# Performance work log

Measured on AMD Instinct MI355X. Metric: run time of the kernel, lower is better.

The kernel has to match this reference:

```python
import jax, jax.numpy as jnp
import numpy as np

D_MODEL = 1024
EXPAND = 2
HEADDIM = 64
D_STATE = 128
D_CONV = 4
D_INNER = EXPAND * D_MODEL          # 2048
NHEADS = D_INNER // HEADDIM         # 32
CONV_DIM = D_INNER + 2 * D_STATE    # x, B, C share the depthwise conv
EPS = 1e-5


def setup_inputs() -> dict:
    key = jax.random.key(0)
    ks = jax.random.split(key, 8)
    d_in_proj = 2 * D_INNER + 2 * D_STATE + NHEADS
    x = jax.random.normal(ks[0], (2, 2048, D_MODEL), jnp.float32)
    W_in = jax.random.normal(ks[1], (D_MODEL, d_in_proj), jnp.float32) * (D_MODEL ** -0.5)
    conv_w = jax.random.normal(ks[2], (CONV_DIM, D_CONV), jnp.float32) * 0.2
    conv_b = jnp.zeros((CONV_DIM,), jnp.float32)
    # dt init: softplus(dt_bias) in [1e-3, 1e-1]  (inverse-softplus init, as in mamba_ssm)
    dt = jnp.exp(jax.random.uniform(ks[3], (NHEADS,), jnp.float32,
                                    minval=np.log(1e-3), maxval=np.log(1e-1)))
    dt_bias = dt + jnp.log(-jnp.expm1(-dt))
    A_log = jnp.log(jax.random.uniform(ks[4], (NHEADS,), jnp.float32, minval=1.0, maxval=16.0))
    D = jnp.ones((NHEADS,), jnp.float32)
    norm_w = jnp.ones((D_INNER,), jnp.float32)
    W_out = jax.random.normal(ks[5], (D_INNER, D_MODEL), jnp.float32) * (D_INNER ** -0.5)
    return dict(x=x, W_in=W_in, conv_w=conv_w, conv_b=conv_b, dt_bias=dt_bias,
                A_log=A_log, D=D, norm_w=norm_w, W_out=W_out)


def _causal_depthwise_conv(u, w, b):
    # u: (B, L, C), w: (C, K) depthwise, causal (pad K-1 on the left)
    B, L, C = u.shape
    up = jnp.pad(u, ((0, 0), (D_CONV - 1, 0), (0, 0)))
    y = b
    for k in range(D_CONV):
        y = y + up[:, k:k + L, :] * w[:, k]
    return y


def _rms(v):
    return v * jax.lax.rsqrt(jnp.mean(v * v, axis=-1, keepdims=True) + EPS)


def reference(x, W_in, conv_w, conv_b, dt_bias, A_log, D, norm_w, W_out):
    b, l, _ = x.shape
    zxbcdt = x @ W_in                                  # (b, l, 2*d_inner + 2*d_state + nheads)
    z = zxbcdt[..., :D_INNER]
    xBC = zxbcdt[..., D_INNER:D_INNER + CONV_DIM]
    dt = jax.nn.softplus(zxbcdt[..., -NHEADS:] + dt_bias)   # (b, l, h)
    xBC = jax.nn.silu(_causal_depthwise_conv(xBC, conv_w, conv_b))
    xs = xBC[..., :D_INNER].reshape(b, l, NHEADS, HEADDIM)  # (b, l, h, p)
    Bm = xBC[..., D_INNER:D_INNER + D_STATE]                 # (b, l, n)
    Cm = xBC[..., D_INNER + D_STATE:]                        # (b, l, n)
    A = -jnp.exp(A_log)                                      # (h,)
    decay = jnp.exp(dt * A)                                  # (b, l, h)

    def step(h, inp):
        dec_t, dt_t, x_t, B_t, C_t = inp   # (b,h) (b,h) (b,h,p) (b,n) (b,n)
        h = h * dec_t[:, :, None, None] + (dt_t[:, :, None] * x_t)[..., None] * B_t[:, None, None, :]
        y_t = jnp.einsum('bhpn,bn->bhp', h, C_t)
        return h, y_t

    h0 = jnp.zeros((b, NHEADS, HEADDIM, D_STATE), x.dtype)
    xs_t = (decay.transpose(1, 0, 2), dt.transpose(1, 0, 2),
            xs.transpose(1, 0, 2, 3), Bm.transpose(1, 0, 2), Cm.transpose(1, 0, 2))
    _, ys = jax.lax.scan(step, h0, xs_t)                     # ys: (l, b, h, p)
    y = ys.transpose(1, 0, 2, 3) + D[None, None, :, None] * xs
    y = y.reshape(b, l, D_INNER)
    # gated RMSNorm (RMSNormGated in mamba_ssm), then out projection
    y = _rms(y * jax.nn.silu(z)) * norm_w
    out = y @ W_out                                          # (b, l, d_model)
    # wrapper: post RMSNorm (weight freshly initialized to ones) + residual
    return _rms(out) + x
```

## Files before the change

### kernel.cpp

```cpp
#include <hip/hip_runtime.h>
#include <hip/hip_bf16.h>

#define DMODEL 1024
#define DI     2048
#define DSTATE 128
#define NH     32
#define HD     64
#define CONVD  2304
#define LSEQ   2048
#define BATCH  2
#define DPROJ  4384
#define NPAD   4480
#define EPSV   1e-5f
#define QCH    128
#define NCH    16

#define AS1 __attribute__((address_space(1)))
#define AS3 __attribute__((address_space(3)))

typedef __attribute__((ext_vector_type(8))) short bf16x8;
typedef __attribute__((ext_vector_type(4))) float f32x4;

union U4 { ushort4 u; __hip_bfloat16 h[4]; };

__device__ __forceinline__ float bf2f(unsigned short u) {
  union { unsigned int i; float f; } c; c.i = ((unsigned)u) << 16; return c.f;
}
__device__ __forceinline__ ushort4 pack4(float x0, float x1, float x2, float x3) {
  U4 p;
  p.h[0] = __float2bfloat16(x0); p.h[1] = __float2bfloat16(x1);
  p.h[2] = __float2bfloat16(x2); p.h[3] = __float2bfloat16(x3);
  return p.u;
}

__device__ __forceinline__ bf16x8 ldsfrag(const __hip_bfloat16* base, int row, int ke) {
  int byte = row * 256 + ke * 2;
  byte ^= (row & 7) << 4;
  return *reinterpret_cast<const bf16x8*>(reinterpret_cast<const char*>(base) + byte);
}
__device__ __forceinline__ void ldswr4(__hip_bfloat16* base, int row, int col4, ushort4 v) {
  int byte = row * 256 + col4 * 2;
  byte ^= (row & 7) << 4;
  *reinterpret_cast<ushort4*>(reinterpret_cast<char*>(base) + byte) = v;
}
__device__ __forceinline__ void ldswr8(__hip_bfloat16* base, int row, int colElem,
                                       unsigned lo, unsigned hi) {
  int byte = row * 256 + colElem * 2;
  byte ^= (row & 7) << 4;
  uint2 v; v.x = lo; v.y = hi;
  *reinterpret_cast<uint2*>(reinterpret_cast<char*>(base) + byte) = v;
}
__device__ __forceinline__ bf16x8 frag32(const __hip_bfloat16* base, int row, int g) {
  int byte = row * 64 + (((g ^ (row >> 1)) & 3) << 4);
  return *reinterpret_cast<const bf16x8*>(reinterpret_cast<const char*>(base) + byte);
}
__device__ __forceinline__ bf16x8 frag64s(const __hip_bfloat16* base, int row, int ch) {
  int byte = row * 128 + ((ch ^ (row & 7)) << 4);
  return *reinterpret_cast<const bf16x8*>(reinterpret_cast<const char*>(base) + byte);
}

__device__ __forceinline__ void quadtr(unsigned a01, unsigned a23, int ql,
                                       unsigned& w01, unsigned& w23) {
  unsigned y01 = __shfl_xor((int)a01, 1), y23 = __shfl_xor((int)a23, 1);
  unsigned c01 = (ql & 1) ? ((y01 >> 16) | (a01 & 0xFFFF0000u))
                          : ((a01 & 0xFFFFu) | (y01 << 16));
  unsigned c23 = (ql & 1) ? ((y23 >> 16) | (a23 & 0xFFFF0000u))
                          : ((a23 & 0xFFFFu) | (y23 << 16));
  unsigned d01 = __shfl_xor((int)c01, 2), d23 = __shfl_xor((int)c23, 2);
  w01 = (ql & 2) ? d23 : c01;
  w23 = (ql & 2) ? c23 : d01;
}


__global__ void f32_to_bf16_kernel(const float* __restrict__ in,
                                   __hip_bfloat16* __restrict__ out, int n4) {
  int i = blockIdx.x * 256 + threadIdx.x;
  if (i >= n4) return;
  float4 v = reinterpret_cast<const float4*>(in)[i];
  reinterpret_cast<ushort4*>(out)[i] = pack4(v.x, v.y, v.z, v.w);
}

__global__ void transpose_f32_bf16(const float* __restrict__ in,
                                   __hip_bfloat16* __restrict__ out,
                                   int R, int C, int Cpad) {
  __shared__ float tile[32][33];
  int n0 = blockIdx.x * 32, k0 = blockIdx.y * 32;
  int tx = threadIdx.x, ty = threadIdx.y;
#pragma unroll
  for (int j = 0; j < 32; j += 8) {
    int k = k0 + ty + j, n = n0 + tx;
    tile[ty + j][tx] = (n < C) ? in[(size_t)k * C + n] : 0.f;
  }
  __syncthreads();
#pragma unroll
  for (int j = 0; j < 32; j += 8) {
    int n = n0 + ty + j, k = k0 + tx;
    if (n < Cpad) out[(size_t)n * R + k] = __float2bfloat16(tile[tx][ty + j]);
  }
}


__global__ __launch_bounds__(512, 2)
void gemm256_bt(const __hip_bfloat16* __restrict__ A,
                const __hip_bfloat16* __restrict__ Bt,
                __hip_bfloat16* __restrict__ C, int K) {
  __shared__ __hip_bfloat16 smA[2][256 * 64];
  __shared__ __hip_bfloat16 smB[2][256 * 64];
  const int xcd = blockIdx.x & 7;
  const int i = blockIdx.x >> 3;
  const int bm = (xcd * 2 + (i & 1)) * 256;
  const int bn = (i >> 1) * 256;
  const int tid = threadIdx.x;
  const int w = tid >> 6, lane = tid & 63;
  const int wm = w >> 2, wn = w & 3;
  const int fr = lane & 15, g = lane >> 4;
  const int srow = w * 8 + (lane >> 3);
  const int scol = ((lane & 7) ^ (lane >> 3)) * 8;

  f32x4 acc[8][4];
#pragma unroll
  for (int m = 0; m < 8; ++m)
#pragma unroll
    for (int n = 0; n < 4; ++n) acc[m][n] = (f32x4){0.f, 0.f, 0.f, 0.f};

  const __hip_bfloat16* aS = A + (size_t)(bm + srow) * K + scol;
  const __hip_bfloat16* bS = Bt + (size_t)(bn + srow) * K + scol;

  auto STAGE = [&](int buf, int kt) {
    const int k0 = kt << 6;
#pragma unroll
    for (int j = 0; j < 4; ++j) {
      __builtin_amdgcn_global_load_lds((const AS1 void*)(aS + (size_t)(j * 64) * K + k0),
                                       (AS3 void*)(&smA[buf][(j * 64 + w * 8) * 64]), 16, 0, 0);
      __builtin_amdgcn_global_load_lds((const AS1 void*)(bS + (size_t)(j * 64) * K + k0),
                                       (AS3 void*)(&smB[buf][(j * 64 + w * 8) * 64]), 16, 0, 0);
    }
  };

  STAGE(0, 0);
  int cur = 0;
  const int nt = K >> 6;
  for (int kt = 0; kt < nt; ++kt) {
    if (kt + 1 < nt) {
      STAGE(cur ^ 1, kt + 1);
      asm volatile("s_waitcnt vmcnt(8)" ::: "memory");
    } else {
      asm volatile("s_waitcnt vmcnt(0)" ::: "memory");
    }
    __builtin_amdgcn_s_barrier();
    __builtin_amdgcn_s_setprio(1);
#pragma unroll
    for (int ks = 0; ks < 2; ++ks) {
      const int ch = ks * 4 + g;
      bf16x8 af[8], bfv[4];
#pragma unroll
      for (int m = 0; m < 8; ++m)
        af[m] = frag64s(&smA[cur][0], wm * 128 + m * 16 + fr, ch);
#pragma unroll
      for (int n = 0; n < 4; ++n)
        bfv[n] = frag64s(&smB[cur][0], wn * 64 + n * 16 + fr, ch);
#pragma unroll
      for (int m = 0; m < 8; ++m)
#pragma unroll
        for (int n = 0; n < 4; ++n)
          acc[m][n] = __builtin_amdgcn_mfma_f32_16x16x32_bf16(af[m], bfv[n], acc[m][n], 0, 0, 0);
    }
    __builtin_amdgcn_s_setprio(0);
    __builtin_amdgcn_s_barrier();
    cur ^= 1;
  }

  const int rb = g * 4;
#pragma unroll
  for (int m = 0; m < 8; ++m)
#pragma unroll
    for (int n = 0; n < 4; ++n) {
      int row = bm + wm * 128 + m * 16 + rb;
      int col = bn + wn * 64 + n * 16 + fr;
      __hip_bfloat16* cp = C + (size_t)row * NPAD + col;
#pragma unroll
      for (int j = 0; j < 4; ++j)
        cp[(size_t)j * NPAD] = __float2bfloat16(acc[m][n][j]);
    }
}


template <int OUTMODE, int SPLITK>
__global__ __launch_bounds__(256, 4)
void gemm_bt3(const __hip_bfloat16* __restrict__ A,
              const __hip_bfloat16* __restrict__ Bt,
              void* __restrict__ Cout0, float* __restrict__ Cout1,
              float* __restrict__ dtraw,
              int M, int N, int K, int bnOff, int NT) {
  __shared__ __hip_bfloat16 smA[2][128 * 32];
  __shared__ __hip_bfloat16 smB[2][128 * 32];
  int bb = blockIdx.x;
  int s = 0;
  if constexpr (SPLITK == 2) { s = bb >> 8; bb &= 255; }
  int bm, bn;
  if (NT == 0) {
    const int xcd = bb & 7;
    const int i = bb >> 3;
    bm = ((xcd << 2) + (i & 3)) * 128;
    bn = bnOff + (i >> 2) * 128;
  } else {
    bm = (bb / NT) * 128;
    bn = bnOff + (bb % NT) * 128;
  }
  const int Kp = (SPLITK == 2) ? (K >> 1) : K;
  const int kbase = s * Kp;
  const int t = threadIdx.x;
  const int w = t >> 6, lane = t & 63;
  const int wr = (w >> 1) * 64, wc = (w & 1) * 64;
  const int fr = lane & 15, g = lane >> 4;
  const int srow = lane >> 2;
  const int scol = ((lane & 3) ^ ((lane >> 3) & 3)) * 8;

  f32x4 acc[4][4];
#pragma unroll
  for (int m = 0; m < 4; ++m)
#pragma unroll
    for (int n = 0; n < 4; ++n) acc[m][n] = (f32x4){0.f, 0.f, 0.f, 0.f};

  const __hip_bfloat16* aSrc = A + (size_t)(bm + srow) * K + kbase + scol;
  const __hip_bfloat16* bSrc = Bt + (size_t)(bn + srow) * K + kbase + scol;

  auto STAGE = [&](int buf, int k0) {
#pragma unroll
    for (int j = 0; j < 2; ++j) {
      int ro = w * 32 + j * 16;
      __builtin_amdgcn_global_load_lds((const AS1 void*)(aSrc + (size_t)ro * K + k0),
                                       (AS3 void*)(&smA[buf][ro * 32]), 16, 0, 0);
      __builtin_amdgcn_global_load_lds((const AS1 void*)(bSrc + (size_t)ro * K + k0),
                                       (AS3 void*)(&smB[buf][ro * 32]), 16, 0, 0);
    }
  };

  STAGE(0, 0);
  __syncthreads();
  const int nt = Kp >> 5;
  int cur = 0;
  for (int kt = 0; kt < nt; ++kt) {
    if (kt + 1 < nt) STAGE(cur ^ 1, (kt + 1) << 5);
    bf16x8 af[4], bfv[4];
#pragma unroll
    for (int m = 0; m < 4; ++m) af[m] = frag32(&smA[cur][0], wr + m * 16 + fr, g);
#pragma unroll
    for (int n = 0; n < 4; ++n) bfv[n] = frag32(&smB[cur][0], wc + n * 16 + fr, g);
#pragma unroll
    for (int m = 0; m < 4; ++m)
#pragma unroll
      for (int n = 0; n < 4; ++n)
        acc[m][n] = __builtin_amdgcn_mfma_f32_16x16x32_bf16(af[m], bfv[n], acc[m][n], 0, 0, 0);
    __syncthreads();
    cur ^= 1;
  }

  const int r4 = g * 4;
  const int cn = lane & 15;
#pragma unroll
  for (int m = 0; m < 4; ++m)
#pragma unroll
    for (int n = 0; n < 4; ++n) {
      int row = bm + wr + m * 16 + r4;
      int col = bn + wc + n * 16 + cn;
      if constexpr (OUTMODE == 0) {
        float* cp = (float*)(s ? Cout1 : (float*)Cout0) + (size_t)row * N + col;
#pragma unroll
        for (int j = 0; j < 4; ++j) cp[(size_t)j * N] = acc[m][n][j];
      } else {
        __hip_bfloat16* cp = (__hip_bfloat16*)Cout0 + (size_t)row * N + col;
#pragma unroll
        for (int j = 0; j < 4; ++j) {
          float v = acc[m][n][j];
          cp[(size_t)j * N] = __float2bfloat16(v);
          if (col >= DI + CONVD && col < DPROJ)
            dtraw[(size_t)(row + j) * NH + (col - (DI + CONVD))] = v;
        }
      }
    }
}


__global__ __launch_bounds__(256)
void chunk_stats_kernel(const float* __restrict__ dtraw, const float* __restrict__ dt_bias,
                        const float* __restrict__ A_log,
                        float* __restrict__ csb, float* __restrict__ dtc,
                        float* __restrict__ swb, float* __restrict__ cumdecb,
                        float* __restrict__ pbuf) {
  int w = threadIdx.x >> 6, lane = threadIdx.x & 63;
  int bid = blockIdx.x * 4 + w;
  int c = bid & (NCH - 1);
  int h = (bid >> 4) & 31;
  int b = bid >> 9;
  int t0 = c * QCH;
  float a = expf(A_log[h]);
  float bias = dt_bias[h];
  const float* dtp = dtraw + ((size_t)b * LSEQ + t0) * NH + h;
  float r0 = dtp[lane * NH] + bias;
  float r1 = dtp[(64 + lane) * NH] + bias;
  float v0 = (r0 > 20.f) ? r0 : log1pf(expf(r0));
  float v1 = (r1 > 20.f) ? r1 : log1pf(expf(r1));
  float s0 = v0;
#pragma unroll
  for (int off = 1; off < 64; off <<= 1) {
    float tv = __shfl_up(s0, off);
    if (lane >= off) s0 += tv;
  }
  float T0 = __shfl(s0, 63);
  float s1 = v1;
#pragma unroll
  for (int off = 1; off < 64; off <<= 1) {
    float tv = __shfl_up(s1, off);
    if (lane >= off) s1 += tv;
  }
  float cs1 = s1 + T0;
  float Tt = __shfl(s1, 63) + T0;
  size_t base = (size_t)bid * 128;
  csb[base + lane] = s0;        csb[base + 64 + lane] = cs1;
  dtc[base + lane] = v0;        dtc[base + 64 + lane] = v1;
  swb[base + lane] = v0 * expf(-a * (Tt - s0));
  swb[base + 64 + lane] = v1 * expf(-a * (Tt - cs1));
  cumdecb[base + lane] = expf(-a * s0);
  cumdecb[base + 64 + lane] = expf(-a * cs1);
  if (lane == 0) pbuf[bid] = expf(-a * Tt);
}


__global__ __launch_bounds__(256)
void conv_silu_kernel(const __hip_bfloat16* __restrict__ zxb,
                      const float* __restrict__ cw,
                      const float* __restrict__ cb,
                      __hip_bfloat16* __restrict__ xbc) {
  int idx = blockIdx.x * 256 + threadIdx.x;
  if (idx >= BATCH * (LSEQ / 4) * (CONVD / 8)) return;
  int c8 = idx % (CONVD / 8);
  int bl4 = idx / (CONVD / 8);
  int l0 = (bl4 % (LSEQ / 4)) * 4;
  int b = bl4 / (LSEQ / 4);
  int c0 = c8 * 8;
  const __hip_bfloat16* src = zxb + (size_t)b * LSEQ * NPAD + DI + c0;

  float wv[8][4];
#pragma unroll
  for (int j = 0; j < 8; ++j)
    *reinterpret_cast<float4*>(wv[j]) = *reinterpret_cast<const float4*>(cw + (c0 + j) * 4);
  float bias[8];
  *reinterpret_cast<float4*>(bias) = *reinterpret_cast<const float4*>(cb + c0);
  *reinterpret_cast<float4*>(bias + 4) = *reinterpret_cast<const float4*>(cb + c0 + 4);

  float hist[7][8];
#pragma unroll
  for (int r = 0; r < 7; ++r) {
    int row = l0 - 3 + r;
    if (row >= 0) {
      uint4 v = *reinterpret_cast<const uint4*>(src + (size_t)row * NPAD);
      unsigned uu[4] = {v.x, v.y, v.z, v.w};
#pragma unroll
      for (int j = 0; j < 8; ++j)
        hist[r][j] = bf2f((j & 1) ? (unsigned short)(uu[j >> 1] >> 16)
                                  : (unsigned short)(uu[j >> 1] & 0xFFFF));
    } else {
#pragma unroll
      for (int j = 0; j < 8; ++j) hist[r][j] = 0.f;
    }
  }

#pragma unroll
  for (int t = 0; t < 4; ++t) {
    float acc[8];
#pragma unroll
    for (int j = 0; j < 8; ++j) {
      float a = bias[j];
      a = fmaf(wv[j][0], hist[t + 0][j], a);
      a = fmaf(wv[j][1], hist[t + 1][j], a);
      a = fmaf(wv[j][2], hist[t + 2][j], a);
      a = fmaf(wv[j][3], hist[t + 3][j], a);
      acc[j] = a / (1.f + expf(-a));
    }
    ushort4* dst = reinterpret_cast<ushort4*>(
        xbc + ((size_t)b * LSEQ + l0 + t) * CONVD + c0);
    dst[0] = pack4(acc[0], acc[1], acc[2], acc[3]);
    dst[1] = pack4(acc[4], acc[5], acc[6], acc[7]);
  }
}


__global__ __launch_bounds__(256, 2)
void ssd_mfma_local(const __hip_bfloat16* __restrict__ bxc,
                    const float* __restrict__ csb, const float* __restrict__ dtc,
                    const float* __restrict__ swb,
                    const float* __restrict__ A_log, const float* __restrict__ Dparm,
                    __hip_bfloat16* __restrict__ y, __hip_bfloat16* __restrict__ sbuf) {
  __shared__ __hip_bfloat16 T_B[128 * 128];
  __shared__ __hip_bfloat16 T_C[128 * 128];
  __shared__ __hip_bfloat16 T_X[64 * 128];

  const int bid = blockIdx.x;
  const int c = bid & (NCH - 1);
  const int h = (bid >> 4) & 31;
  const int b = bid >> 9;
  const int tid = threadIdx.x;
  const int w = tid >> 6, lane = tid & 63;
  const int q = lane >> 2, ql = lane & 3;
  const int t0 = c * QCH;
  const __hip_bfloat16* xc = bxc + (size_t)b * LSEQ * CONVD;
  const float a = expf(A_log[h]);
  const float Dh = Dparm[h];

  {
    const int rsub = lane >> 4;
    const int ch = lane & 15;
#pragma unroll
    for (int j = 0; j < 8; ++j) {
      int row = w * 32 + j * 4 + rsub;
      int sc_ = ch ^ (row & 7);
      const __hip_bfloat16* pB = xc + (size_t)(t0 + row) * CONVD + DI + sc_ * 8;
      __builtin_amdgcn_global_load_lds((const AS1 void*)pB,
                                       (AS3 void*)(T_B + (w * 32 + j * 4) * 128), 16, 0, 0);
      __builtin_amdgcn_global_load_lds((const AS1 void*)(pB + DSTATE),
                                       (AS3 void*)(T_C + (w * 32 + j * 4) * 128), 16, 0, 0);
    }
  }
#pragma unroll
  for (int r = 0; r < 8; ++r) {
    int gidx = w * 128 + q * 8 + r;
    int tb = (gidx & 31) * 4;
    int pb = (gidx >> 5) * 4;
    int t = tb + ql;
    ushort4 xv = *reinterpret_cast<const ushort4*>(xc + (size_t)(t0 + t) * CONVD + h * HD + pb);
    unsigned a01 = (unsigned)xv.x | ((unsigned)xv.y << 16);
    unsigned a23 = (unsigned)xv.z | ((unsigned)xv.w << 16);
    unsigned w01, w23;
    quadtr(a01, a23, ql, w01, w23);
    ldswr8(T_X, pb + ql, tb, w01, w23);
  }
  __syncthreads();

  const int fr = lane & 15;
  const int fk = (lane >> 4) * 8;
  const int rb = (lane >> 4) * 4;

  const int sR0 = (w >> 1) * 64, tC0 = (w & 1) * 64;
  f32x4 g[4][4];
#pragma unroll
  for (int m = 0; m < 4; ++m)
#pragma unroll
    for (int n = 0; n < 4; ++n) g[m][n] = (f32x4){0.f, 0.f, 0.f, 0.f};
  for (int kk = 0; kk < 128; kk += 32) {
    bf16x8 af[4], bfv[4];
#pragma unroll
    for (int m = 0; m < 4; ++m) af[m] = ldsfrag(T_B, sR0 + m * 16 + fr, kk + fk);
#pragma unroll
    for (int n = 0; n < 4; ++n) bfv[n] = ldsfrag(T_C, tC0 + n * 16 + fr, kk + fk);
#pragma unroll
    for (int m = 0; m < 4; ++m)
#pragma unroll
      for (int n = 0; n < 4; ++n)
        g[m][n] = __builtin_amdgcn_mfma_f32_16x16x32_bf16(af[m], bfv[n], g[m][n], 0, 0, 0);
  }
  __syncthreads();

  {
    const float* csp = csb + (size_t)bid * 128;
    const float* dtp = dtc + (size_t)bid * 128;
#pragma unroll
    for (int m = 0; m < 4; ++m) {
      int sb0 = sR0 + m * 16 + rb;
      float cs_s[4], dt_s[4];
#pragma unroll
      for (int j = 0; j < 4; ++j) { cs_s[j] = csp[sb0 + j]; dt_s[j] = dtp[sb0 + j]; }
#pragma unroll
      for (int n = 0; n < 4; ++n) {
        int tt = tC0 + n * 16 + fr;
        float cst = csp[tt];
        float vv[4];
#pragma unroll
        for (int j = 0; j < 4; ++j) {
          int s = sb0 + j;
          float e = __expf(-a * (cst - cs_s[j])) * dt_s[j];
          float pv = (s <= tt) ? g[m][n][j] * e : 0.f;
          vv[j] = pv + ((s == tt) ? Dh : 0.f);
        }
        ldswr4(T_B, tt, sb0, pack4(vv[0], vv[1], vv[2], vv[3]));
      }
    }
    const float* swp = swb + (size_t)bid * 128;
#pragma unroll
    for (int r = 0; r < 16; ++r) {
      int gidx = w * 256 + q * 16 + r;
      int tb = (gidx & 31) * 4;
      int nb = (gidx >> 5) * 4;
      int t = tb + ql;
      ushort4 bv = *reinterpret_cast<const ushort4*>(xc + (size_t)(t0 + t) * CONVD + DI + nb);
      float wt = swp[t];
      ushort4 sv = pack4(bf2f(bv.x) * wt, bf2f(bv.y) * wt, bf2f(bv.z) * wt, bf2f(bv.w) * wt);
      unsigned a01 = (unsigned)sv.x | ((unsigned)sv.y << 16);
      unsigned a23 = (unsigned)sv.z | ((unsigned)sv.w << 16);
      unsigned w01, w23;
      quadtr(a01, a23, ql, w01, w23);
      ldswr8(T_C, nb + ql, tb, w01, w23);
    }
  }
  __syncthreads();

  {
    int tR0 = w * 32;
    f32x4 yac[2][4];
#pragma unroll
    for (int m = 0; m < 2; ++m)
#pragma unroll
      for (int n = 0; n < 4; ++n) yac[m][n] = (f32x4){0.f, 0.f, 0.f, 0.f};
    for (int kk = 0; kk < 128; kk += 32) {
      bf16x8 af[2], bfv[4];
#pragma unroll
      for (int m = 0; m < 2; ++m) af[m] = ldsfrag(T_B, tR0 + m * 16 + fr, kk + fk);
#pragma unroll
      for (int n = 0; n < 4; ++n) bfv[n] = ldsfrag(T_X, n * 16 + fr, kk + fk);
#pragma unroll
      for (int m = 0; m < 2; ++m)
#pragma unroll
        for (int n = 0; n < 4; ++n)
          yac[m][n] = __builtin_amdgcn_mfma_f32_16x16x32_bf16(af[m], bfv[n], yac[m][n], 0, 0, 0);
    }
#pragma unroll
    for (int m = 0; m < 2; ++m)
#pragma unroll
      for (int n = 0; n < 4; ++n) {
        int trow = tR0 + m * 16 + rb;
        int pc = n * 16 + fr;
        __hip_bfloat16* yp = y + ((size_t)b * LSEQ + t0 + trow) * DI + h * HD + pc;
#pragma unroll
        for (int j = 0; j < 4; ++j)
          yp[(size_t)j * DI] = __float2bfloat16(yac[m][n][j]);
      }
  }

  {
    int pR0 = (w >> 1) * 32, nC0 = (w & 1) * 64;
    f32x4 sac[2][4];
#pragma unroll
    for (int m = 0; m < 2; ++m)
#pragma unroll
      for (int n = 0; n < 4; ++n) sac[m][n] = (f32x4){0.f, 0.f, 0.f, 0.f};
    for (int kk = 0; kk < 128; kk += 32) {
      bf16x8 af[2], bfv[4];
#pragma unroll
      for (int m = 0; m < 2; ++m) af[m] = ldsfrag(T_X, pR0 + m * 16 + fr, kk + fk);
#pragma unroll
      for (int n = 0; n < 4; ++n) bfv[n] = ldsfrag(T_C, nC0 + n * 16 + fr, kk + fk);
#pragma unroll
      for (int m = 0; m < 2; ++m)
#pragma unroll
        for (int n = 0; n < 4; ++n)
          sac[m][n] = __builtin_amdgcn_mfma_f32_16x16x32_bf16(af[m], bfv[n], sac[m][n], 0, 0, 0);
    }
    __hip_bfloat16* sg = sbuf + (size_t)bid * 8192;
#pragma unroll
    for (int m = 0; m < 2; ++m)
#pragma unroll
      for (int n = 0; n < 4; ++n) {
        int p = pR0 + m * 16 + rb;
        int nn = nC0 + n * 16 + fr;
#pragma unroll
        for (int j = 0; j < 4; ++j)
          sg[(size_t)(p + j) * 128 + nn] = __float2bfloat16(sac[m][n][j]);
      }
  }
}


__global__ void ssd_prop_kernel(__hip_bfloat16* __restrict__ sbuf,
                                const float* __restrict__ pbuf) {
  int idx = blockIdx.x * 256 + threadIdx.x;
  int bh = idx >> 13;
  int e = idx & 8191;
  __hip_bfloat16* base = sbuf + (size_t)bh * NCH * 8192 + e;
  const float* pb = pbuf + bh * NCH;
  float hs = 0.f;
  for (int cc = 0; cc < NCH; ++cc) {
    float sc = __bfloat162float(base[(size_t)cc * 8192]);
    base[(size_t)cc * 8192] = __float2bfloat16(hs);
    hs = fmaf(hs, pb[cc], sc);
  }
}


__global__ __launch_bounds__(256, 4)
void ssd_mfma_corr(const __hip_bfloat16* __restrict__ bxc, const __hip_bfloat16* __restrict__ sbuf,
                   const float* __restrict__ cumdecb, __hip_bfloat16* __restrict__ y) {
  const int bid = (blockIdx.x / 15) * 16 + 1 + (blockIdx.x % 15);
  const int h = (bid >> 4) & 31;
  const int b = bid >> 9;
  const int tid = threadIdx.x;
  const int w = tid >> 6, lane = tid & 63;
  const int t0 = (bid & (NCH - 1)) * QCH;
  const __hip_bfloat16* xc = bxc + (size_t)b * LSEQ * CONVD;
  const __hip_bfloat16* hsb = sbuf + (size_t)bid * 8192;
  const int fr = lane & 15;
  const int fk = (lane >> 4) * 8;
  const int rb = (lane >> 4) * 4;
  const int tR0 = w * 32;

  f32x4 ac[2][4];
#pragma unroll
  for (int m = 0; m < 2; ++m)
#pragma unroll
    for (int n = 0; n < 4; ++n) ac[m][n] = (f32x4){0.f, 0.f, 0.f, 0.f};

#pragma unroll
  for (int kk = 0; kk < 128; kk += 32) {
    bf16x8 af[2], bfv[4];
#pragma unroll
    for (int m = 0; m < 2; ++m)
      af[m] = *reinterpret_cast<const bf16x8*>(
          xc + (size_t)(t0 + tR0 + m * 16 + fr) * CONVD + DI + DSTATE + kk + fk);
#pragma unroll
    for (int n = 0; n < 4; ++n)
      bfv[n] = *reinterpret_cast<const bf16x8*>(hsb + (size_t)(n * 16 + fr) * 128 + kk + fk);
#pragma unroll
    for (int m = 0; m < 2; ++m)
#pragma unroll
      for (int n = 0; n < 4; ++n)
        ac[m][n] = __builtin_amdgcn_mfma_f32_16x16x32_bf16(af[m], bfv[n], ac[m][n], 0, 0, 0);
  }

  const float* cdp = cumdecb + (size_t)bid * 128;
#pragma unroll
  for (int m = 0; m < 2; ++m) {
    int trow = tR0 + m * 16 + rb;
    float cd[4];
#pragma unroll
    for (int j = 0; j < 4; ++j) cd[j] = cdp[trow + j];
#pragma unroll
    for (int n = 0; n < 4; ++n) {
      int pc = n * 16 + fr;
      __hip_bfloat16* yp = y + ((size_t)b * LSEQ + t0 + trow) * DI + h * HD + pc;
#pragma unroll
      for (int j = 0; j < 4; ++j) {
        float old = __bfloat162float(yp[(size_t)j * DI]);
        yp[(size_t)j * DI] = __float2bfloat16(old + cd[j] * ac[m][n][j]);
      }
    }
  }
}


__global__ __launch_bounds__(256)
void gate_rms_kernel(const __hip_bfloat16* __restrict__ y, const __hip_bfloat16* __restrict__ zxb,
                     const float* __restrict__ nw, __hip_bfloat16* __restrict__ g) {
  int row = blockIdx.x;
  int t = threadIdx.x;
  int c0 = t * 8;
  const __hip_bfloat16* yr = y + (size_t)row * DI + c0;
  const __hip_bfloat16* zr = zxb + (size_t)row * NPAD + c0;
  ushort4 y0 = *reinterpret_cast<const ushort4*>(yr);
  ushort4 y1 = *reinterpret_cast<const ushort4*>(yr + 4);
  ushort4 z0 = *reinterpret_cast<const ushort4*>(zr);
  ushort4 z1 = *reinterpret_cast<const ushort4*>(zr + 4);
  float zf[8] = {bf2f(z0.x), bf2f(z0.y), bf2f(z0.z), bf2f(z0.w),
                 bf2f(z1.x), bf2f(z1.y), bf2f(z1.z), bf2f(z1.w)};
  float yf[8] = {bf2f(y0.x), bf2f(y0.y), bf2f(y0.z), bf2f(y0.w),
                 bf2f(y1.x), bf2f(y1.y), bf2f(y1.z), bf2f(y1.w)};
  float v[8];
  float ss = 0.f;
#pragma unroll
  for (int j = 0; j < 8; ++j) {
    float z = zf[j];
    float vv = yf[j] * (z / (1.f + expf(-z)));
    v[j] = vv;
    ss += vv * vv;
  }
#pragma unroll
  for (int off = 32; off; off >>= 1) ss += __shfl_down(ss, off);
  __shared__ float red[4];
  if ((t & 63) == 0) red[t >> 6] = ss;
  __syncthreads();
  float tot = red[0] + red[1] + red[2] + red[3];
  float rstd = rsqrtf(tot * (1.f / DI) + EPSV);
  float4 na = *reinterpret_cast<const float4*>(nw + c0);
  float4 nb = *reinterpret_cast<const float4*>(nw + c0 + 4);
  ushort4 o0 = pack4(v[0] * rstd * na.x, v[1] * rstd * na.y,
                     v[2] * rstd * na.z, v[3] * rstd * na.w);
  ushort4 o1v = pack4(v[4] * rstd * nb.x, v[5] * rstd * nb.y,
                      v[6] * rstd * nb.z, v[7] * rstd * nb.w);
  ushort4* gp = reinterpret_cast<ushort4*>(g + (size_t)row * DI + c0);
  gp[0] = o0;
  gp[1] = o1v;
}


__global__ __launch_bounds__(256)
void final_rms_add(const float* __restrict__ o1a, const float* __restrict__ o1b,
                   const float* __restrict__ x, float* __restrict__ out) {
  int row = blockIdx.x;
  int t = threadIdx.x;
  int c0 = t * 4;
  float4 oa = *reinterpret_cast<const float4*>(o1a + (size_t)row * DMODEL + c0);
  float4 ob = *reinterpret_cast<const float4*>(o1b + (size_t)row * DMODEL + c0);
  float4 o;
  o.x = oa.x + ob.x; o.y = oa.y + ob.y; o.z = oa.z + ob.z; o.w = oa.w + ob.w;
  float ss = o.x * o.x + o.y * o.y + o.z * o.z + o.w * o.w;
#pragma unroll
  for (int off = 32; off; off >>= 1) ss += __shfl_down(ss, off);
  __shared__ float red[4];
  if ((t & 63) == 0) red[t >> 6] = ss;
  __syncthreads();
  float tot = red[0] + red[1] + red[2] + red[3];
  float rstd = rsqrtf(tot * (1.f / DMODEL) + EPSV);
  float4 xv = *reinterpret_cast<const float4*>(x + (size_t)row * DMODEL + c0);
  float4 r;
  r.x = o.x * rstd + xv.x;
  r.y = o.y * rstd + xv.y;
  r.z = o.z * rstd + xv.z;
  r.w = o.w * rstd + xv.w;
  *reinterpret_cast<float4*>(out + (size_t)row * DMODEL + c0) = r;
}


extern "C" void kernel_launch(void* const* d_in, const int* in_sizes, int n_in,
                              void* d_out, int out_size, void* d_ws, size_t ws_size,
                              hipStream_t stream) {
  const float* x       = (const float*)d_in[0];
  const float* W_in    = (const float*)d_in[1];
  const float* conv_w  = (const float*)d_in[2];
  const float* conv_b  = (const float*)d_in[3];
  const float* dt_bias = (const float*)d_in[4];
  const float* A_log   = (const float*)d_in[5];
  const float* Dp      = (const float*)d_in[6];
  const float* norm_w  = (const float*)d_in[7];
  const float* W_out   = (const float*)d_in[8];
  float* out = (float*)d_out;

  float* zxF  = (float*)d_ws;
  __hip_bfloat16* zxb = (__hip_bfloat16*)zxF;
  float* xbcF = zxF + (size_t)18350080;
  __hip_bfloat16* xbc = (__hip_bfloat16*)xbcF;
  float* ybufF = xbcF + (size_t)9437184;
  __hip_bfloat16* ybuf = (__hip_bfloat16*)ybufF;
  float* dtraw = ybufF + (size_t)8388608;
  float* cumdecb = dtraw + (size_t)131072;
  __hip_bfloat16* xbf   = (__hip_bfloat16*)(cumdecb + 131072);
  __hip_bfloat16* wtin  = xbf + (size_t)4194304;
  __hip_bfloat16* wtout = wtin + (size_t)4587520;
  float* pbuf = (float*)(wtout + (size_t)2097152);
  float* csb  = pbuf + 1024;
  float* dtc  = csb + (size_t)131072;
  float* swb  = dtc + (size_t)131072;
  __hip_bfloat16* sbuf = xbf;
  __hip_bfloat16* gbf = xbf;
  float* o1a = xbcF;
  float* o1b = xbcF + (size_t)4194304;

  f32_to_bf16_kernel<<<4096, 256, 0, stream>>>(x, xbf, 1048576);
  transpose_f32_bf16<<<dim3(140, 32), dim3(32, 8), 0, stream>>>(W_in, wtin, 1024, 4384, 4480);
  transpose_f32_bf16<<<dim3(32, 64), dim3(32, 8), 0, stream>>>(W_out, wtout, 2048, 1024, 1024);

  gemm256_bt<<<256, 512, 0, stream>>>(xbf, wtin, zxb, 1024);
  gemm_bt3<1, 1><<<96, 256, 0, stream>>>(xbf, wtin, (void*)zxb, nullptr, dtraw,
                                         4096, NPAD, 1024, 4096, 3);

  chunk_stats_kernel<<<256, 256, 0, stream>>>(dtraw, dt_bias, A_log, csb, dtc, swb, cumdecb, pbuf);
  conv_silu_kernel<<<1152, 256, 0, stream>>>(zxb, conv_w, conv_b, xbc);

  ssd_mfma_local<<<1024, 256, 0, stream>>>(xbc, csb, dtc, swb, A_log, Dp, ybuf, sbuf);
  ssd_prop_kernel<<<2048, 256, 0, stream>>>(sbuf, pbuf);
  ssd_mfma_corr<<<960, 256, 0, stream>>>(xbc, sbuf, cumdecb, ybuf);

  gate_rms_kernel<<<4096, 256, 0, stream>>>(ybuf, zxb, norm_w, gbf);

  gemm_bt3<0, 2><<<512, 256, 0, stream>>>(gbf, wtout, (void*)o1a, o1b, nullptr,
                                          4096, 1024, 2048, 0, 0);

  final_rms_add<<<4096, 256, 0, stream>>>(o1a, o1b, x, out);
}
```

Measured before the change: 207.1 us.

## Deepen in_proj GEMM pipeline to four K=32 stages and drop trailing barrier

The in-projection GEMM now uses four LDS buffers of K=32 slices instead of two buffers of K=64, and prefetches two stages ahead. Because a buffer is not overwritten until two iterations after it is read, the second barrier per iteration is removed. The aim is to hide global-to-LDS latency better and cut synchronisation. The cost is twice as many loop iterations and barriers per unit of K, plus a new swizzle (frag32) for the narrower tiles.

```diff
diff --git a/kernel.cpp b/kernel.cpp
--- a/kernel.cpp
+++ b/kernel.cpp
@@ -54,10 +54,6 @@
   int byte = row * 64 + (((g ^ (row >> 1)) & 3) << 4);
   return *reinterpret_cast<const bf16x8*>(reinterpret_cast<const char*>(base) + byte);
 }
-__device__ __forceinline__ bf16x8 frag64s(const __hip_bfloat16* base, int row, int ch) {
-  int byte = row * 128 + ((ch ^ (row & 7)) << 4);
-  return *reinterpret_cast<const bf16x8*>(reinterpret_cast<const char*>(base) + byte);
-}
 
 __device__ __forceinline__ void quadtr(unsigned a01, unsigned a23, int ql,
                                        unsigned& w01, unsigned& w23) {
@@ -104,8 +100,8 @@
 void gemm256_bt(const __hip_bfloat16* __restrict__ A,
                 const __hip_bfloat16* __restrict__ Bt,
                 __hip_bfloat16* __restrict__ C, int K) {
-  __shared__ __hip_bfloat16 smA[2][256 * 64];
-  __shared__ __hip_bfloat16 smB[2][256 * 64];
+  __shared__ __hip_bfloat16 smA[4][256 * 32];
+  __shared__ __hip_bfloat16 smB[4][256 * 32];
   const int xcd = blockIdx.x & 7;
   const int i = blockIdx.x >> 3;
   const int bm = (xcd * 2 + (i & 1)) * 256;
@@ -114,8 +110,8 @@
   const int w = tid >> 6, lane = tid & 63;
   const int wm = w >> 2, wn = w & 3;
   const int fr = lane & 15, g = lane >> 4;
-  const int srow = w * 8 + (lane >> 3);
-  const int scol = ((lane & 7) ^ (lane >> 3)) * 8;
+  const int srow = tid >> 2;
+  const int sc = (((tid & 3) ^ ((srow >> 1) & 3)) << 3);
 
   f32x4 acc[8][4];
 #pragma unroll
@@ -123,51 +119,49 @@
 #pragma unroll
     for (int n = 0; n < 4; ++n) acc[m][n] = (f32x4){0.f, 0.f, 0.f, 0.f};
 
-  const __hip_bfloat16* aS = A + (size_t)(bm + srow) * K + scol;
-  const __hip_bfloat16* bS = Bt + (size_t)(bn + srow) * K + scol;
+  const __hip_bfloat16* aS = A + (size_t)(bm + srow) * K + sc;
+  const __hip_bfloat16* bS = Bt + (size_t)(bn + srow) * K + sc;
+  const int dbase = w * 512;
 
   auto STAGE = [&](int buf, int kt) {
-    const int k0 = kt << 6;
-#pragma unroll
-    for (int j = 0; j < 4; ++j) {
-      __builtin_amdgcn_global_load_lds((const AS1 void*)(aS + (size_t)(j * 64) * K + k0),
-                                       (AS3 void*)(&smA[buf][(j * 64 + w * 8) * 64]), 16, 0, 0);
-      __builtin_amdgcn_global_load_lds((const AS1 void*)(bS + (size_t)(j * 64) * K + k0),
-                                       (AS3 void*)(&smB[buf][(j * 64 + w * 8) * 64]), 16, 0, 0);
+    const int k0 = kt << 5;
+#pragma unroll
+    for (int j = 0; j < 2; ++j) {
+      __builtin_amdgcn_global_load_lds((const AS1 void*)(aS + (size_t)(j * 128) * K + k0),
+                                       (AS3 void*)(&smA[buf][j * 4096 + dbase]), 16, 0, 0);
+      __builtin_amdgcn_global_load_lds((const AS1 void*)(bS + (size_t)(j * 128) * K + k0),
+                                       (AS3 void*)(&smB[buf][j * 4096 + dbase]), 16, 0, 0);
     }
   };
 
+  const int nt = K >> 5;
   STAGE(0, 0);
-  int cur = 0;
-  const int nt = K >> 6;
+  STAGE(1, 1);
   for (int kt = 0; kt < nt; ++kt) {
-    if (kt + 1 < nt) {
-      STAGE(cur ^ 1, kt + 1);
+    const int cur = kt & 3;
+    if (kt + 2 < nt) {
+      STAGE((kt + 2) & 3, kt + 2);
       asm volatile("s_waitcnt vmcnt(8)" ::: "memory");
+    } else if (kt + 1 < nt) {
+      asm volatile("s_waitcnt vmcnt(4)" ::: "memory");
     } else {
       asm volatile("s_waitcnt vmcnt(0)" ::: "memory");
     }
     __builtin_amdgcn_s_barrier();
     __builtin_amdgcn_s_setprio(1);
-#pragma unroll
-    for (int ks = 0; ks < 2; ++ks) {
-      const int ch = ks * 4 + g;
-      bf16x8 af[8], bfv[4];
-#pragma unroll
-      for (int m = 0; m < 8; ++m)
-        af[m] = frag64s(&smA[cur][0], wm * 128 + m * 16 + fr, ch);
+    bf16x8 af[8], bfv[4];
+#pragma unroll
+    for (int m = 0; m < 8; ++m)
+      af[m] = frag32(&smA[cur][0], wm * 128 + m * 16 + fr, g);
+#pragma unroll
+    for (int n = 0; n < 4; ++n)
+      bfv[n] = frag32(&smB[cur][0], wn * 64 + n * 16 + fr, g);
+#pragma unroll
+    for (int m = 0; m < 8; ++m)
 #pragma unroll
       for (int n = 0; n < 4; ++n)
-        bfv[n] = frag64s(&smB[cur][0], wn * 64 + n * 16 + fr, ch);
-#pragma unroll
-      for (int m = 0; m < 8; ++m)
-#pragma unroll
-        for (int n = 0; n < 4; ++n)
-          acc[m][n] = __builtin_amdgcn_mfma_f32_16x16x32_bf16(af[m], bfv[n], acc[m][n], 0, 0, 0);
-    }
+        acc[m][n] = __builtin_amdgcn_mfma_f32_16x16x32_bf16(af[m], bfv[n], acc[m][n], 0, 0, 0);
     __builtin_amdgcn_s_setprio(0);
-    __builtin_amdgcn_s_barrier();
-    cur ^= 1;
   }
 
   const int rb = g * 4;
```

Result: no change. 203.2 us (-1.9%).
